# Kernel tuning notes

Hardware: AMD Instinct MI355X
Metric: run time of the kernel (lower is better)

## Reference

```python
import jax, jax.numpy as jnp
import numpy as np

B, K2, C, H, W = 8, 9, 1, 256, 1216


def setup_inputs() -> dict:
    key = jax.random.key(0)
    k1, k2 = jax.random.split(key)
    affinity = jax.random.normal(k1, (B, K2, H, W), dtype=jnp.float32)
    feature = jax.random.normal(k2, (B, C, H, W), dtype=jnp.float32)
    return {"affinity": affinity, "feature": feature, "times": 24}


def reference(affinity, feature, times):
    # affinity: [B, 9, H, W]; feature: [B, C, H, W]
    b, k2, h, w = affinity.shape
    a_abs = jnp.abs(affinity)
    a_norm = a_abs / a_abs.sum(axis=1, keepdims=True)  # per-pixel normalized weights [B,9,H,W]

    def step(feat, _):
        fp = jnp.pad(feat, ((0, 0), (0, 0), (1, 1), (1, 1)))  # 3x3 stencil, pad=1
        # Stack the 9 shifted views: [B, 9, C, H, W] (row-major over 3x3 window,
        # matching index = pad_h*3 + pad_w in the torch loop)
        shifts = jnp.stack(
            [fp[:, :, i:i + h, j:j + w] for i in range(3) for j in range(3)],
            axis=1,
        )
        out = jnp.einsum('bncij,bnij->bcij', shifts, a_norm)
        return out, None

    feat, _ = jax.lax.scan(step, feature, None, length=times)
    return feat
```

## Files before the change

### kernel.cpp

```cpp
#include <hip/hip_runtime.h>

#define BB 8
#define HH 256
#define WW 1216
#define TIMES 24

#define KF 4
#define TSZ 26
#define FSZ 34
#define NT 512
#define NFPIX (FSZ*FSZ)
#define TGX 47
#define TGY 10
#define NTILES (TGX*TGY)

#define WPIX 1024
#define WELEM (9*WPIX)
#define WBYTES (WELEM*2)
#define WCHUNKS (WBYTES/256)

static const size_t HW = (size_t)HH * WW;
#define DEQ (1.0f/65535.0f)

typedef float f32x2 __attribute__((ext_vector_type(2)));

#define LDS_BARRIER() do { asm volatile("s_waitcnt lgkmcnt(0)" ::: "memory"); \
                           __builtin_amdgcn_s_barrier(); } while (0)

__device__ __forceinline__ unsigned lds_off(const void* p) {
    return (unsigned)(size_t)(const __attribute__((address_space(3))) void*)p;
}

__device__ __forceinline__ void gload_lds4(const unsigned int* g, void* l) {
    __builtin_amdgcn_global_load_lds(
        (const __attribute__((address_space(1))) void*)g,
        (__attribute__((address_space(3))) void*)l, 4, 0, 0);
}

#define STEPV(BC, o0, o1) do {                                                        \
    unsigned _ab = lds_off((BC) + tb0);                                               \
    f32x2 _v0,_v1,_v2,_v3,_v4,_v5;                                                    \
    asm volatile("ds_read2_b32 %0, %1 offset0:0   offset1:1"  : "=v"(_v0) : "v"(_ab));\
    asm volatile("ds_read2_b32 %0, %1 offset0:2   offset1:34" : "=v"(_v1) : "v"(_ab));\
    asm volatile("ds_read2_b32 %0, %1 offset0:35  offset1:36" : "=v"(_v2) : "v"(_ab));\
    asm volatile("ds_read2_b32 %0, %1 offset0:68  offset1:69" : "=v"(_v3) : "v"(_ab));\
    asm volatile("ds_read2_b32 %0, %1 offset0:70  offset1:102": "=v"(_v4) : "v"(_ab));\
    asm volatile("ds_read2_b32 %0, %1 offset0:103 offset1:104": "=v"(_v5) : "v"(_ab));\
    asm volatile("s_waitcnt lgkmcnt(0)" ::: "memory");                                \
    __builtin_amdgcn_sched_barrier(0);                                                \
    float _t00=_v0.x,_t01=_v0.y,_t02=_v1.x;                                           \
    float _t10=_v1.y,_t11=_v2.x,_t12=_v2.y;                                           \
    float _t20=_v3.x,_t21=_v3.y,_t22=_v4.x;                                           \
    float _t30=_v4.y,_t31=_v5.x,_t32=_v5.y;                                           \
    (o0) = w0[0]*_t00+w0[1]*_t01+w0[2]*_t02 + w0[3]*_t10+w0[4]*_t11+w0[5]*_t12        \
         + w0[6]*_t20+w0[7]*_t21+w0[8]*_t22;                                          \
    (o1) = w1[0]*_t10+w1[1]*_t11+w1[2]*_t12 + w1[3]*_t20+w1[4]*_t21+w1[5]*_t22        \
         + w1[6]*_t30+w1[7]*_t31+w1[8]*_t32;                                          \
} while (0)

#define STORE2(BN) do {                                                               \
    asm volatile("ds_write2_b32 %0, %1, %2 offset0:0 offset1:34"                      \
        :: "v"(lds_off((BN) + cw0)), "v"(r0), "v"(r1) : "memory");                    \
} while (0)

template <bool FIRST>
__global__ __launch_bounds__(NT, 4) void fused4_kernel(unsigned int* __restrict__ wq,
                                                       const float* __restrict__ aff,
                                                       const float* __restrict__ src,
                                                       float* __restrict__ dst) {
    __shared__ float S[NFPIX], P[NFPIX], Q[NFPIX];
    __shared__ unsigned int Wl[WELEM / 2];

    const int t    = threadIdx.x;
    const int wv   = t >> 6;
    const int lane = t & 63;
    const int tile = blockIdx.x;
    const int ty   = tile / TGX, tx = tile - ty * TGX;
    const int x0   = tx * TSZ,   y0 = ty * TSZ;

    const int wx  = t & 31;
    const int wy0 = (t >> 5) * 2;
    const int gx  = x0 - (KF - 1) + wx;
    const int gy0 = y0 - (KF - 1) + wy0;
    const int gy1 = gy0 + 1;
    const bool in0 = (unsigned)gy0 < (unsigned)HH && (unsigned)gx < (unsigned)WW;
    const bool in1 = (unsigned)gy1 < (unsigned)HH && (unsigned)gx < (unsigned)WW;
    const long woff0 = (long)gy0 * WW + gx;
    const long woff1 = (long)gy1 * WW + gx;
    const int  tb0 = wy0 * FSZ + wx;
    const int  cw0 = (wy0 + 1) * FSZ + (wx + 1);
    const int  widx = (t >> 5) * 32 + (t & 31);

    int foff[3]; bool fok[3];
#pragma unroll
    for (int r = 0; r < 3; ++r) {
        int p  = t + r * NT;
        int fy = p / FSZ, fx = p - fy * FSZ;
        int gfy = y0 - KF + fy, gfx = x0 - KF + fx;
        fok[r]  = (p < NFPIX) && (unsigned)gfy < (unsigned)HH && (unsigned)gfx < (unsigned)WW;
        foff[r] = gfy * WW + gfx;
    }

#pragma unroll
    for (int r = 0; r < 3; ++r) {
        int p = t + r * NT;
        if (p < NFPIX) { P[p] = 0.0f; Q[p] = 0.0f; }
    }

    float a0[9], a1[9];
    if (!FIRST) {
        const unsigned int* w32 = wq + (size_t)(tile * BB) * (WELEM / 2);
        for (int c = wv; c < WCHUNKS; c += 8)
            gload_lds4(w32 + c * 64 + lane, (char*)Wl + c * 256);
    } else {
#pragma unroll
        for (int n = 0; n < 9; ++n) {
            a0[n] = in0 ? aff[woff0 + (long)n * (long)HW] : 0.0f;
            a1[n] = in1 ? aff[woff1 + (long)n * (long)HW] : 0.0f;
        }
    }
#pragma unroll
    for (int r = 0; r < 3; ++r) {
        int p = t + r * NT;
        if (p < NFPIX) S[p] = fok[r] ? src[foff[r]] : 0.0f;
    }
    __syncthreads();

    for (int b = 0; b < BB; ++b) {
        float w0[9], w1[9];
        if (!FIRST) {
#pragma unroll
            for (int n = 0; n < 9; ++n) {
                unsigned u = Wl[n * (WPIX / 2) + widx];
                w0[n] = (float)(u & 0xffffu) * DEQ;
                w1[n] = (float)(u >> 16)     * DEQ;
            }
        } else {
            int qi0[9], qi1[9];
            {
                float s0 = 0.0f, s1 = 0.0f;
#pragma unroll
                for (int n = 0; n < 9; ++n) {
                    a0[n] = fabsf(a0[n]); s0 += a0[n];
                    a1[n] = fabsf(a1[n]); s1 += a1[n];
                }
                float sc0 = in0 ? (65535.0f / s0) : 0.0f;
                float sc1 = in1 ? (65535.0f / s1) : 0.0f;
                int tot0 = 0, tot1 = 0, m0 = 0, m1 = 0;
                float vm0 = a0[0], vm1 = a1[0];
#pragma unroll
                for (int n = 0; n < 9; ++n) {
                    qi0[n] = (int)(a0[n] * sc0 + 0.5f); tot0 += qi0[n];
                    qi1[n] = (int)(a1[n] * sc1 + 0.5f); tot1 += qi1[n];
                    if (a0[n] > vm0) { vm0 = a0[n]; m0 = n; }
                    if (a1[n] > vm1) { vm1 = a1[n]; m1 = n; }
                }
                int d0 = 65535 - tot0, d1 = 65535 - tot1;
#pragma unroll
                for (int n = 0; n < 9; ++n) {
                    qi0[n] += (in0 && n == m0) ? d0 : 0;
                    qi1[n] += (in1 && n == m1) ? d1 : 0;
                }
            }
            unsigned int* rec = wq + (size_t)(tile * BB + b) * (WELEM / 2);
#pragma unroll
            for (int n = 0; n < 9; ++n) {
                rec[n * (WPIX / 2) + widx] =
                    (unsigned)qi0[n] | ((unsigned)qi1[n] << 16);
                w0[n] = (float)qi0[n] * DEQ;
                w1[n] = (float)qi1[n] * DEQ;
            }
        }
        LDS_BARRIER();

        const bool pf = (b + 1 < BB);
        float fn[3], an0[9], an1[9];
        if (pf) {
            if (!FIRST) {
                const unsigned int* w32 =
                    wq + (size_t)(tile * BB + b + 1) * (WELEM / 2);
                for (int c = wv; c < WCHUNKS; c += 8)
                    gload_lds4(w32 + c * 64 + lane, (char*)Wl + c * 256);
            } else {
                const float* ap = aff + (size_t)(b + 1) * 9 * HW;
#pragma unroll
                for (int n = 0; n < 9; ++n) {
                    an0[n] = in0 ? ap[woff0 + (long)n * (long)HW] : 0.0f;
                    an1[n] = in1 ? ap[woff1 + (long)n * (long)HW] : 0.0f;
                }
            }
            const float* sp = src + (size_t)(b + 1) * HW;
#pragma unroll
            for (int r = 0; r < 3; ++r) fn[r] = fok[r] ? sp[foff[r]] : 0.0f;
        }
        __builtin_amdgcn_sched_barrier(0);

        float r0, r1;
        STEPV(S, r0, r1);
        STORE2(P);
        LDS_BARRIER();
        STEPV(P, r0, r1);
        STORE2(Q);
        LDS_BARRIER();
        if (pf) {
#pragma unroll
            for (int r = 0; r < 3; ++r) {
                int p = t + r * NT;
                if (p < NFPIX) S[p] = fn[r];
            }
        }
        STEPV(Q, r0, r1);
        STORE2(P);
        LDS_BARRIER();
        STEPV(P, r0, r1);

        if (FIRST && pf) {
#pragma unroll
            for (int n = 0; n < 9; ++n) { a0[n] = an0[n]; a1[n] = an1[n]; }
        }

        asm volatile("s_waitcnt vmcnt(0)" ::: "memory");
        LDS_BARRIER();

        const size_t base = (size_t)b * HW;
        if ((unsigned)(wx - (KF - 1)) < (unsigned)TSZ) {
            if ((unsigned)(wy0     - (KF - 1)) < (unsigned)TSZ && in0)
                dst[base + (size_t)gy0 * WW + gx] = r0;
            if ((unsigned)(wy0 + 1 - (KF - 1)) < (unsigned)TSZ && in1)
                dst[base + (size_t)gy1 * WW + gx] = r1;
        }
    }
}

extern "C" void kernel_launch(void* const* d_in, const int* in_sizes, int n_in,
                              void* d_out, int out_size, void* d_ws, size_t ws_size,
                              hipStream_t stream) {
    const float* affinity = (const float*)d_in[0];
    const float* feature  = (const float*)d_in[1];

    unsigned int* wq = (unsigned int*)d_ws;
    float* bufA = (float*)((char*)d_ws + (size_t)NTILES * BB * WBYTES);
    float* bufO = (float*)d_out;

    fused4_kernel<true><<<dim3(NTILES), dim3(NT), 0, stream>>>(
        wq, affinity, feature, bufA);

    const float* src = bufA;
    for (int l = 1; l < TIMES / KF; ++l) {
        float* dst = (l & 1) ? bufO : bufA;
        fused4_kernel<false><<<dim3(NTILES), dim3(NT), 0, stream>>>(
            wq, affinity, src, dst);
        src = dst;
    }
}
```

Measured before the change: 166.9 us.

## Drop ninth quantized weight plane and double-buffer weight records in LDS

Stores only 8 of the 9 quantized 16-bit weight planes per pixel pair, rebuilding the ninth as 65535 minus the sum, since the quantized weights sum exactly to 65535. This cuts the weight-record traffic to global memory and LDS by about one ninth. The LDS weight buffer becomes a two-slot double buffer so the prefetch of the next batch's weights can go to the other slot, which lets the barrier that guarded the single buffer be removed. The cost is more LDS space and a few extra integer adds per pixel.

```diff
diff --git a/kernel.cpp b/kernel.cpp
--- a/kernel.cpp
+++ b/kernel.cpp
@@ -14,9 +14,8 @@
 #define TGY 10
 #define NTILES (TGX*TGY)
 
-#define WPIX 1024
-#define WELEM (9*WPIX)
-#define WBYTES (WELEM*2)
+#define WRECD 4096
+#define WBYTES (WRECD*4)
 #define WCHUNKS (WBYTES/256)
 
 static const size_t HW = (size_t)HH * WW;
@@ -69,7 +68,7 @@
                                                        const float* __restrict__ src,
                                                        float* __restrict__ dst) {
     __shared__ float S[NFPIX], P[NFPIX], Q[NFPIX];
-    __shared__ unsigned int Wl[WELEM / 2];
+    __shared__ unsigned int Wl[2][WRECD];
 
     const int t    = threadIdx.x;
     const int wv   = t >> 6;
@@ -109,9 +108,9 @@
 
     float a0[9], a1[9];
     if (!FIRST) {
-        const unsigned int* w32 = wq + (size_t)(tile * BB) * (WELEM / 2);
+        const unsigned int* w32 = wq + (size_t)(tile * BB) * WRECD;
         for (int c = wv; c < WCHUNKS; c += 8)
-            gload_lds4(w32 + c * 64 + lane, (char*)Wl + c * 256);
+            gload_lds4(w32 + c * 64 + lane, (char*)&Wl[0][0] + c * 256);
     } else {
 #pragma unroll
         for (int n = 0; n < 9; ++n) {
@@ -127,14 +126,22 @@
     __syncthreads();
 
     for (int b = 0; b < BB; ++b) {
+        const int cur = b & 1;
         float w0[9], w1[9];
         if (!FIRST) {
-#pragma unroll
-            for (int n = 0; n < 9; ++n) {
-                unsigned u = Wl[n * (WPIX / 2) + widx];
-                w0[n] = (float)(u & 0xffffu) * DEQ;
-                w1[n] = (float)(u >> 16)     * DEQ;
-            }
+            unsigned s0i = 0, s1i = 0;
+#pragma unroll
+            for (int n = 0; n < 8; ++n) {
+                unsigned u  = Wl[cur][n * 512 + widx];
+                unsigned lo = u & 0xffffu, hi = u >> 16;
+                w0[n] = (float)lo * DEQ;
+                w1[n] = (float)hi * DEQ;
+                s0i += lo; s1i += hi;
+            }
+            unsigned q80 = in0 ? (65535u - s0i) : 0u;
+            unsigned q81 = in1 ? (65535u - s1i) : 0u;
+            w0[8] = (float)q80 * DEQ;
+            w1[8] = (float)q81 * DEQ;
         } else {
             int qi0[9], qi1[9];
             {
@@ -162,25 +169,26 @@
                     qi1[n] += (in1 && n == m1) ? d1 : 0;
                 }
             }
-            unsigned int* rec = wq + (size_t)(tile * BB + b) * (WELEM / 2);
+            unsigned int* rec = wq + (size_t)(tile * BB + b) * WRECD;
+#pragma unroll
+            for (int n = 0; n < 8; ++n)
+                rec[n * 512 + widx] = (unsigned)qi0[n] | ((unsigned)qi1[n] << 16);
 #pragma unroll
             for (int n = 0; n < 9; ++n) {
-                rec[n * (WPIX / 2) + widx] =
-                    (unsigned)qi0[n] | ((unsigned)qi1[n] << 16);
                 w0[n] = (float)qi0[n] * DEQ;
                 w1[n] = (float)qi1[n] * DEQ;
             }
         }
-        LDS_BARRIER();
 
         const bool pf = (b + 1 < BB);
         float fn[3], an0[9], an1[9];
         if (pf) {
             if (!FIRST) {
                 const unsigned int* w32 =
-                    wq + (size_t)(tile * BB + b + 1) * (WELEM / 2);
+                    wq + (size_t)(tile * BB + b + 1) * WRECD;
                 for (int c = wv; c < WCHUNKS; c += 8)
-                    gload_lds4(w32 + c * 64 + lane, (char*)Wl + c * 256);
+                    gload_lds4(w32 + c * 64 + lane,
+                               (char*)&Wl[cur ^ 1][0] + c * 256);
             } else {
                 const float* ap = aff + (size_t)(b + 1) * 9 * HW;
 #pragma unroll
```

After: 159.2 us (median of 2 runs). 4.6% less time.
